# Performance work log

Hardware: AMD Instinct MI355X
Metric: run time of the kernel (lower is better)

Reference implementation:

```python
import jax, jax.numpy as jnp
import numpy as np

B, CIN, COUT, G = 1, 64, 64, 1
NLAT, NLON = 256, 512
LMAX, MMAX = NLAT, NLON // 2 + 1  # torch-harmonics: lmax=nlat, mmax=nlon//2+1


def _legpoly(mmax, lmax, cost):
    """Fully (ortho) normalized associated Legendre \bar P_l^m(cos t), shape [mmax, lmax, nlat]."""
    nlat = cost.shape[0]
    p = np.zeros((mmax, lmax, nlat), dtype=np.float64)
    sint = np.sqrt(1.0 - cost * cost)
    pmm = np.full(nlat, np.sqrt(1.0 / (4.0 * np.pi)))  # \bar P_0^0
    for m in range(mmax):
        if m < lmax:
            p[m, m] = pmm
        if m + 1 < lmax:
            p[m, m + 1] = np.sqrt(2.0 * m + 3.0) * cost * pmm
        for l in range(m + 2, lmax):
            a = np.sqrt((4.0 * l * l - 1.0) / (l * l - m * m))
            b = np.sqrt(((l - 1.0) ** 2 - m * m) / (4.0 * (l - 1.0) ** 2 - 1.0))
            p[m, l] = a * (cost * p[m, l - 1] - b * p[m, l - 2])
        # diagonal step: \bar P_{m+1}^{m+1}
        pmm = -np.sqrt((2.0 * m + 3.0) / (2.0 * m + 2.0)) * sint * pmm
    return p


def setup_inputs():
    key = jax.random.key(0)
    k1, k2, k3 = jax.random.split(key, 3)
    # Gauss-Legendre nodes/weights (grid='legendre-gauss')
    cost, wq = np.polynomial.legendre.leggauss(NLAT)
    pct = _legpoly(MMAX, LMAX, cost)                      # [m, l, k] - ISHT matrix
    sht_w = pct * wq[None, None, :]                        # [m, l, k] - SHT matrix (Legendre * quadrature)
    x = jax.random.normal(k1, (B, CIN, NLAT, NLON), jnp.float32)
    # weight init: scale = sqrt(1/(Cin/g)), scale[0] *= sqrt(2); complex randn has var 1/2 per component
    scale = np.full(LMAX, np.sqrt(1.0 / (CIN // G)), np.float32)
    scale[0] *= np.sqrt(2.0)
    scale = scale * np.sqrt(0.5)
    weight_r = jax.random.normal(k2, (G, CIN // G, COUT // G, LMAX), jnp.float32) * scale
    weight_i = jax.random.normal(k3, (G, CIN // G, COUT // G, LMAX), jnp.float32) * scale
    return {"x": x, "weight_r": weight_r, "weight_i": weight_i,
            "pct": jnp.asarray(pct.astype(np.float32)),
            "sht_w": jnp.asarray(sht_w.astype(np.float32))}


def reference(x, weight_r, weight_i, pct, sht_w):
    residual = x  # scale_residual is False (same in/out shape and grid)
    x = x.astype(jnp.float32)
    # --- forward real SHT: rfft over lon, Legendre transform over lat ---
    xf = 2.0 * jnp.pi * jnp.fft.rfft(x, axis=-1, norm="forward")          # [B,C,k,m] complex64
    coeffs = jnp.einsum('bckm,mlk->bclm', xf, sht_w.astype(xf.dtype))      # [B,C,l,m]
    Bd, C, L, M = coeffs.shape
    # --- grouped per-l complex weight contraction (_contract_lwise) ---
    w = (weight_r + 1j * weight_i).astype(coeffs.dtype)                    # [g,i,o,l]
    xg = coeffs.reshape(Bd, G, C // G, L, M)
    out = jnp.einsum('bgilm,giol->bgolm', xg, w).reshape(Bd, COUT, L, M)
    # --- inverse real SHT ---
    xk = jnp.einsum('bolm,mlk->bokm', out, pct.astype(out.dtype))          # [B,Cout,k,m]
    y = jnp.fft.irfft(xk, n=NLON, axis=-1, norm="forward")                 # [B,Cout,nlat,nlon]
    return (y.astype(residual.dtype), residual)
```

## Files before the change

kernel.cpp:

```cpp
#include <hip/hip_runtime.h>

typedef _Float16 f16;
typedef _Float16 h8 __attribute__((ext_vector_type(8)));
typedef float f4 __attribute__((ext_vector_type(4)));

#define NLON 512
#define NLAT 256
#define NC   64
#define NM   256
#define NL   256
#define RTOT (NC*NLAT)

#define BO_FTR 0
#define BO_FTI (BO_FTR + 262144)
#define BO_GR  (BO_FTI + 262144)
#define BO_GI  (BO_GR  + 262144)
#define BO_WTR (BO_GI  + 262144)
#define BO_WTI (BO_WTR + 2097152)
#define BO_XFRE (BO_WTI + 2097152)
#define BO_XFIM (BO_XFRE + 8388608)
#define BO_PRE  (BO_XFIM + 8388608)
#define BO_PIM  (BO_PRE + 8388608)
#define BO_QRE  (BO_PIM + 8388608)
#define BO_QIM  (BO_QRE + 8388608)

__device__ inline f4 mfma16(h8 a, h8 b, f4 c) {
  return __builtin_amdgcn_mfma_f32_16x16x32_f16(a, b, c, 0, 0, 0);
}

__global__ void k_tables_h(f16* __restrict__ Ftr, f16* __restrict__ Fti,
                           f16* __restrict__ Gr, f16* __restrict__ Gi) {
  int idx = blockIdx.x * blockDim.x + threadIdx.x;
  if (idx >= NLON * NM) return;
  const float step = 3.14159265358979323846f / 256.0f;
  {
    int m = idx >> 9, n = idx & 511;
    int t = (n * m) & (NLON - 1);
    float th = t * step;
    const float sc = 6.2831853071795864769f / 512.0f;
    Ftr[idx] = (f16)(sc * cosf(th));
    Fti[idx] = (f16)(-sc * sinf(th));
  }
  {
    int n = idx >> 8, m = idx & 255;
    int t = (n * m) & (NLON - 1);
    float th = t * step;
    float s = (m == 0) ? 1.0f : 2.0f;
    Gr[idx] = (f16)(s * cosf(th));
    Gi[idx] = (f16)(-s * sinf(th));
  }
}

__global__ void k_permw2(const float* __restrict__ wr, const float* __restrict__ wi,
                         f16* __restrict__ wTr, f16* __restrict__ wTi) {
  __shared__ float tile[32][33];
  int z = blockIdx.z;
  int o = z >> 1;
  const float* w = (z & 1) ? wi : wr;
  f16* wT = (z & 1) ? wTi : wTr;
  int i0 = blockIdx.y * 32;
  int l0 = blockIdx.x * 32;
  int xx = threadIdx.x, yy = threadIdx.y;
  for (int j = 0; j < 32; j += 8)
    tile[yy + j][xx] = w[(size_t)(i0 + yy + j) * (NC * NL) + (size_t)o * NL + l0 + xx];
  __syncthreads();
  for (int j = 0; j < 32; j += 8)
    wT[(size_t)(l0 + yy + j) * (NC * NC) + (size_t)o * NC + i0 + xx] = (f16)tile[xx][yy + j];
}

__global__ __launch_bounds__(256) void k_s1(
    const float* __restrict__ x, const f16* __restrict__ Ftr,
    const f16* __restrict__ Fti, f16* __restrict__ XFre, f16* __restrict__ XFim,
    float* __restrict__ res) {
  __shared__ f16 Ar[128 * 72], Ai[128 * 72], Bx[64 * 72];
  int t = threadIdx.x;
  int m0 = blockIdx.x * 128, r0 = blockIdx.y * 64;
  int lane = t & 63, w = t >> 6;
  int wm = (w >> 1) * 32, wn = (w & 1) * 32;
  int fr = lane & 15, kg = (lane >> 4) * 8;
  int srow = t >> 2, skc = (t & 3) * 16;
  f4 aR[4][2] = {}, aI[4][2] = {};
  for (int n0 = 0; n0 < NLON; n0 += 64) {
#pragma unroll
    for (int rep = 0; rep < 4; ++rep) {
      int f = rep * 256 + t;
      int row = f >> 3, c8 = (f & 7) * 8;
      *(h8*)&Ar[row * 72 + c8] = *(const h8*)(Ftr + (size_t)(m0 + row) * NLON + n0 + c8);
      *(h8*)&Ai[row * 72 + c8] = *(const h8*)(Fti + (size_t)(m0 + row) * NLON + n0 + c8);
    }
    const float* px = x + (size_t)(r0 + srow) * NLON + n0 + skc;
    float4 v0 = *(const float4*)px;
    float4 v1 = *(const float4*)(px + 4);
    float4 v2 = *(const float4*)(px + 8);
    float4 v3 = *(const float4*)(px + 12);
    if (blockIdx.x == 0) {
      float* pr = res + (size_t)(r0 + srow) * NLON + n0 + skc;
      *(float4*)pr = v0; *(float4*)(pr + 4) = v1;
      *(float4*)(pr + 8) = v2; *(float4*)(pr + 12) = v3;
    }
    h8 h0 = {(f16)v0.x, (f16)v0.y, (f16)v0.z, (f16)v0.w,
             (f16)v1.x, (f16)v1.y, (f16)v1.z, (f16)v1.w};
    h8 h1 = {(f16)v2.x, (f16)v2.y, (f16)v2.z, (f16)v2.w,
             (f16)v3.x, (f16)v3.y, (f16)v3.z, (f16)v3.w};
    *(h8*)&Bx[srow * 72 + skc] = h0;
    *(h8*)&Bx[srow * 72 + skc + 8] = h1;
    __syncthreads();
#pragma unroll
    for (int ks = 0; ks < 64; ks += 32) {
      h8 b0 = *(h8*)&Bx[(wn + fr) * 72 + ks + kg];
      h8 b1 = *(h8*)&Bx[(wn + 16 + fr) * 72 + ks + kg];
#pragma unroll
      for (int im = 0; im < 4; ++im) {
        int mrow = wm + (im >> 1) * 64 + (im & 1) * 16 + fr;
        h8 a = *(h8*)&Ar[mrow * 72 + ks + kg];
        h8 c = *(h8*)&Ai[mrow * 72 + ks + kg];
        aR[im][0] = mfma16(a, b0, aR[im][0]); aR[im][1] = mfma16(a, b1, aR[im][1]);
        aI[im][0] = mfma16(c, b0, aI[im][0]); aI[im][1] = mfma16(c, b1, aI[im][1]);
      }
    }
    __syncthreads();
  }
  int drow = (lane >> 4) * 4, dcol = lane & 15;
#pragma unroll
  for (int im = 0; im < 4; ++im)
#pragma unroll
    for (int j = 0; j < 2; ++j)
#pragma unroll
      for (int b = 0; b < 4; ++b) {
        int mg = m0 + wm + (im >> 1) * 64 + (im & 1) * 16 + drow + b;
        size_t o = (size_t)mg * RTOT + r0 + wn + j * 16 + dcol;
        XFre[o] = (f16)aR[im][j][b];
        XFim[o] = (f16)aI[im][j][b];
      }
}

__global__ __launch_bounds__(256) void k_s2(
    const f16* __restrict__ XFre, const f16* __restrict__ XFim,
    const float* __restrict__ shtw, f16* __restrict__ Pre, f16* __restrict__ Pim) {
  int m = blockIdx.y;
  int l0 = blockIdx.x * 64;
  int t = threadIdx.x;
  if (l0 + 64 <= m) return;
  __shared__ f16 SH[9216];
  f16* Ar = SH;
  f16* Ai = SH + 2560;
  f16* Bs = SH + 5120;
  int lane = t & 63, w = t >> 6;
  int wm = (w >> 1) * 32, wn = (w & 1) * 32;
  int fr = lane & 15, kg = (lane >> 4) * 8;
  int srow = t >> 2, skc = (t & 3) * 8;
  const f16* Abr = XFre + (size_t)m * RTOT;
  const f16* Abi = XFim + (size_t)m * RTOT;
  const float* Bb = shtw + (size_t)m * (NL * NLAT);
  f4 aR[2][2] = {}, aI[2][2] = {};
  for (int k0 = 0; k0 < NLAT; k0 += 32) {
    *(h8*)&Ar[srow * 40 + skc] = *(const h8*)(Abr + (size_t)srow * NLAT + k0 + skc);
    *(h8*)&Ai[srow * 40 + skc] = *(const h8*)(Abi + (size_t)srow * NLAT + k0 + skc);
    const float* pb = Bb + (size_t)(l0 + srow) * NLAT + k0 + skc;
    float4 v0 = *(const float4*)pb;
    float4 v1 = *(const float4*)(pb + 4);
    h8 hb = {(f16)v0.x, (f16)v0.y, (f16)v0.z, (f16)v0.w,
             (f16)v1.x, (f16)v1.y, (f16)v1.z, (f16)v1.w};
    *(h8*)&Bs[srow * 40 + skc] = hb;
    __syncthreads();
    h8 a0 = *(h8*)&Ar[(wm + fr) * 40 + kg],      a1 = *(h8*)&Ar[(wm + 16 + fr) * 40 + kg];
    h8 c0 = *(h8*)&Ai[(wm + fr) * 40 + kg],      c1 = *(h8*)&Ai[(wm + 16 + fr) * 40 + kg];
    h8 b0 = *(h8*)&Bs[(wn + fr) * 40 + kg],      b1 = *(h8*)&Bs[(wn + 16 + fr) * 40 + kg];
    aR[0][0] = mfma16(a0, b0, aR[0][0]); aR[0][1] = mfma16(a0, b1, aR[0][1]);
    aR[1][0] = mfma16(a1, b0, aR[1][0]); aR[1][1] = mfma16(a1, b1, aR[1][1]);
    aI[0][0] = mfma16(c0, b0, aI[0][0]); aI[0][1] = mfma16(c0, b1, aI[0][1]);
    aI[1][0] = mfma16(c1, b0, aI[1][0]); aI[1][1] = mfma16(c1, b1, aI[1][1]);
    __syncthreads();
  }
  f16* Tr = SH;
  f16* Ti = SH + 4608;
  int drow = (lane >> 4) * 4, dcol = lane & 15;
#pragma unroll
  for (int i = 0; i < 2; ++i)
#pragma unroll
    for (int j = 0; j < 2; ++j)
#pragma unroll
      for (int b = 0; b < 4; ++b) {
        int c = wm + i * 16 + drow + b;
        int l = wn + j * 16 + dcol;
        Tr[l * 72 + c] = (f16)aR[i][j][b];
        Ti[l * 72 + c] = (f16)aI[i][j][b];
      }
  __syncthreads();
#pragma unroll
  for (int rep = 0; rep < 4; ++rep) {
    int f = rep * 256 + t;
    int buf = f >> 9, idx = f & 511;
    int ll = idx >> 3, c8 = (idx & 7) * 8;
    const f16* T = buf ? Ti : Tr;
    h8 v = *(const h8*)&T[ll * 72 + c8];
    f16* Pd = buf ? Pim : Pre;
    *(h8*)(Pd + (size_t)(l0 + ll) * RTOT + (size_t)m * 64 + c8) = v;
  }
}

__global__ __launch_bounds__(256) void k_s3(
    const f16* __restrict__ Pre, const f16* __restrict__ Pim,
    const f16* __restrict__ wTr, const f16* __restrict__ wTi,
    f16* __restrict__ Qre, f16* __restrict__ Qim) {
  int l = blockIdx.y;
  int m0 = blockIdx.x * 64;
  int t = threadIdx.x;
  size_t obase = (size_t)l * RTOT + (size_t)m0 * 64;
  if (m0 > l) return;
  __shared__ f16 SH[18432];
  f16* Ar = SH;
  f16* Ai = SH + 4608;
  f16* Br = SH + 9216;
  f16* Bi = SH + 13824;
  const f16* Pbr = Pre + (size_t)l * RTOT + (size_t)m0 * 64;
  const f16* Pbi = Pim + (size_t)l * RTOT + (size_t)m0 * 64;
  const f16* Wbr = wTr + (size_t)l * 4096;
  const f16* Wbi = wTi + (size_t)l * 4096;
#pragma unroll
  for (int rep = 0; rep < 2; ++rep) {
    int f = rep * 256 + t;
    int row = f >> 3, c8 = (f & 7) * 8;
    *(h8*)&Ar[row * 72 + c8] = *(const h8*)(Pbr + (size_t)row * 64 + c8);
    *(h8*)&Ai[row * 72 + c8] = *(const h8*)(Pbi + (size_t)row * 64 + c8);
    *(h8*)&Br[row * 72 + c8] = *(const h8*)(Wbr + (size_t)f * 8);
    *(h8*)&Bi[row * 72 + c8] = *(const h8*)(Wbi + (size_t)f * 8);
  }
  __syncthreads();
  int lane = t & 63, w = t >> 6;
  int wm = (w >> 1) * 32, wn = (w & 1) * 32;
  int fr = lane & 15, kg = (lane >> 4) * 8;
  f4 RR[2][2] = {}, II[2][2] = {}, RI[2][2] = {}, IR[2][2] = {};
#pragma unroll
  for (int ks = 0; ks < 64; ks += 32) {
    h8 a0 = *(h8*)&Ar[(wm + fr) * 72 + ks + kg];
    h8 a1 = *(h8*)&Ar[(wm + 16 + fr) * 72 + ks + kg];
    h8 c0 = *(h8*)&Ai[(wm + fr) * 72 + ks + kg];
    h8 c1 = *(h8*)&Ai[(wm + 16 + fr) * 72 + ks + kg];
    h8 b0 = *(h8*)&Br[(wn + fr) * 72 + ks + kg];
    h8 b1 = *(h8*)&Br[(wn + 16 + fr) * 72 + ks + kg];
    h8 d0 = *(h8*)&Bi[(wn + fr) * 72 + ks + kg];
    h8 d1 = *(h8*)&Bi[(wn + 16 + fr) * 72 + ks + kg];
    RR[0][0] = mfma16(a0, b0, RR[0][0]); RR[0][1] = mfma16(a0, b1, RR[0][1]);
    RR[1][0] = mfma16(a1, b0, RR[1][0]); RR[1][1] = mfma16(a1, b1, RR[1][1]);
    II[0][0] = mfma16(c0, d0, II[0][0]); II[0][1] = mfma16(c0, d1, II[0][1]);
    II[1][0] = mfma16(c1, d0, II[1][0]); II[1][1] = mfma16(c1, d1, II[1][1]);
    RI[0][0] = mfma16(a0, d0, RI[0][0]); RI[0][1] = mfma16(a0, d1, RI[0][1]);
    RI[1][0] = mfma16(a1, d0, RI[1][0]); RI[1][1] = mfma16(a1, d1, RI[1][1]);
    IR[0][0] = mfma16(c0, b0, IR[0][0]); IR[0][1] = mfma16(c0, b1, IR[0][1]);
    IR[1][0] = mfma16(c1, b0, IR[1][0]); IR[1][1] = mfma16(c1, b1, IR[1][1]);
  }
  __syncthreads();
  f16* Tr = SH;
  f16* Ti = SH + 4608;
  int drow = (lane >> 4) * 4, dcol = lane & 15;
#pragma unroll
  for (int i = 0; i < 2; ++i)
#pragma unroll
    for (int j = 0; j < 2; ++j)
#pragma unroll
      for (int b = 0; b < 4; ++b) {
        int mm = wm + i * 16 + drow + b;
        int oo = wn + j * 16 + dcol;
        Tr[mm * 72 + oo] = (f16)(RR[i][j][b] - II[i][j][b]);
        Ti[mm * 72 + oo] = (f16)(RI[i][j][b] + IR[i][j][b]);
      }
  __syncthreads();
#pragma unroll
  for (int rep = 0; rep < 4; ++rep) {
    int f = rep * 256 + t;
    int buf = f >> 9, idx = f & 511;
    int mm = idx >> 3, o8 = (idx & 7) * 8;
    const f16* T = buf ? Ti : Tr;
    h8 v = *(const h8*)&T[mm * 72 + o8];
    f16* Qd = buf ? Qim : Qre;
    *(h8*)(Qd + obase + (size_t)mm * 64 + o8) = v;
  }
}

__global__ __launch_bounds__(256) void k_s4(
    const f16* __restrict__ Qre, const f16* __restrict__ Qim,
    const float* __restrict__ pct, f16* __restrict__ XKre, f16* __restrict__ XKim) {
  __shared__ f16 As[32 * 66], Ais[32 * 66], Bs0[32 * 66], Bs1[32 * 66];
  int m = blockIdx.y;
  int k0b = blockIdx.x * 128;
  int t = threadIdx.x;
  int lane = t & 63, w = t >> 6;
  int wm = (w >> 1) * 32, wn = (w & 1) * 32;
  int fr = lane & 15, kg = (lane >> 4) * 8;
  int lr = t >> 3, c8 = (t & 7) * 8;
  const float* Bb = pct + (size_t)m * (NL * NLAT);
  f4 aR[2][4] = {}, aI[2][4] = {};
  int lstart = m & ~31;
  for (int l0 = lstart; l0 < NL; l0 += 32) {
    *(h8*)&As[lr * 66 + c8]  = *(const h8*)(Qre + (size_t)(l0 + lr) * RTOT + (size_t)m * 64 + c8);
    *(h8*)&Ais[lr * 66 + c8] = *(const h8*)(Qim + (size_t)(l0 + lr) * RTOT + (size_t)m * 64 + c8);
    const float* pb = Bb + (size_t)(l0 + lr) * NLAT + k0b + c8;
    {
      float4 v0 = *(const float4*)pb;
      float4 v1 = *(const float4*)(pb + 4);
      h8 hb = {(f16)v0.x, (f16)v0.y, (f16)v0.z, (f16)v0.w,
               (f16)v1.x, (f16)v1.y, (f16)v1.z, (f16)v1.w};
      *(h8*)&Bs0[lr * 66 + c8] = hb;
    }
    {
      float4 v0 = *(const float4*)(pb + 64);
      float4 v1 = *(const float4*)(pb + 68);
      h8 hb = {(f16)v0.x, (f16)v0.y, (f16)v0.z, (f16)v0.w,
               (f16)v1.x, (f16)v1.y, (f16)v1.z, (f16)v1.w};
      *(h8*)&Bs1[lr * 66 + c8] = hb;
    }
    __syncthreads();
    h8 a0, a1, c0, c1, b0, b1, b2, b3;
#pragma unroll
    for (int e = 0; e < 8; ++e) {
      int row = (kg + e) * 66;
      a0[e] = As[row + wm + fr];
      a1[e] = As[row + wm + 16 + fr];
      c0[e] = Ais[row + wm + fr];
      c1[e] = Ais[row + wm + 16 + fr];
      b0[e] = Bs0[row + wn + fr];
      b1[e] = Bs0[row + wn + 16 + fr];
      b2[e] = Bs1[row + wn + fr];
      b3[e] = Bs1[row + wn + 16 + fr];
    }
    aR[0][0] = mfma16(a0, b0, aR[0][0]); aR[0][1] = mfma16(a0, b1, aR[0][1]);
    aR[0][2] = mfma16(a0, b2, aR[0][2]); aR[0][3] = mfma16(a0, b3, aR[0][3]);
    aR[1][0] = mfma16(a1, b0, aR[1][0]); aR[1][1] = mfma16(a1, b1, aR[1][1]);
    aR[1][2] = mfma16(a1, b2, aR[1][2]); aR[1][3] = mfma16(a1, b3, aR[1][3]);
    aI[0][0] = mfma16(c0, b0, aI[0][0]); aI[0][1] = mfma16(c0, b1, aI[0][1]);
    aI[0][2] = mfma16(c0, b2, aI[0][2]); aI[0][3] = mfma16(c0, b3, aI[0][3]);
    aI[1][0] = mfma16(c1, b0, aI[1][0]); aI[1][1] = mfma16(c1, b1, aI[1][1]);
    aI[1][2] = mfma16(c1, b2, aI[1][2]); aI[1][3] = mfma16(c1, b3, aI[1][3]);
    __syncthreads();
  }
  int drow = (lane >> 4) * 4, dcol = lane & 15;
#pragma unroll
  for (int i = 0; i < 2; ++i)
#pragma unroll
    for (int j = 0; j < 4; ++j)
#pragma unroll
      for (int b = 0; b < 4; ++b) {
        int orow = wm + i * 16 + drow + b;
        int kcol = k0b + (j >> 1) * 64 + (j & 1) * 16 + wn + dcol;
        size_t o = (size_t)m * RTOT + (size_t)orow * NLAT + kcol;
        XKre[o] = (f16)aR[i][j][b];
        XKim[o] = (f16)aI[i][j][b];
      }
}

__global__ __launch_bounds__(256) void k_s5(
    const f16* __restrict__ XKre, const f16* __restrict__ XKim,
    const f16* __restrict__ Gr, const f16* __restrict__ Gi,
    float* __restrict__ y) {
  __shared__ f16 Ar[32 * 66], Ai[32 * 66], Br[128 * 34], Bi[128 * 34];
  int t = threadIdx.x;
  int n0 = blockIdx.x * 128, r0 = blockIdx.y * 64;
  int lane = t & 63, w = t >> 6;
  int wm = (w >> 1) * 32, wn = (w & 1) * 32;
  int fr = lane & 15, kg = (lane >> 4) * 8;
  int mr = t >> 3, r8 = (t & 7) * 8;
  f4 acc[2][4] = {};
  for (int m0 = 0; m0 < NM; m0 += 32) {
    *(h8*)&Ar[mr * 66 + r8] = *(const h8*)(XKre + (size_t)(m0 + mr) * RTOT + r0 + r8);
    *(h8*)&Ai[mr * 66 + r8] = *(const h8*)(XKim + (size_t)(m0 + mr) * RTOT + r0 + r8);
#pragma unroll
    for (int rep = 0; rep < 2; ++rep) {
      int f = rep * 256 + t;
      int row = f >> 2, cc = (f & 3) * 8;
      *(h8*)&Br[row * 34 + cc] = *(const h8*)(Gr + (size_t)(n0 + row) * NM + m0 + cc);
      *(h8*)&Bi[row * 34 + cc] = *(const h8*)(Gi + (size_t)(n0 + row) * NM + m0 + cc);
    }
    __syncthreads();
    h8 a0, a1, c0, c1;
#pragma unroll
    for (int e = 0; e < 8; ++e) {
      int row = (kg + e) * 66;
      a0[e] = Ar[row + wm + fr];
      a1[e] = Ar[row + wm + 16 + fr];
      c0[e] = Ai[row + wm + fr];
      c1[e] = Ai[row + wm + 16 + fr];
    }
#pragma unroll
    for (int j = 0; j < 4; ++j) {
      int nb = wn + (j & 1) * 16 + (j >> 1) * 64;
      h8 b = *(h8*)&Br[(nb + fr) * 34 + kg];
      h8 d = *(h8*)&Bi[(nb + fr) * 34 + kg];
      acc[0][j] = mfma16(a0, b, acc[0][j]);
      acc[1][j] = mfma16(a1, b, acc[1][j]);
      acc[0][j] = mfma16(c0, d, acc[0][j]);
      acc[1][j] = mfma16(c1, d, acc[1][j]);
    }
    __syncthreads();
  }
  int drow = (lane >> 4) * 4, dcol = lane & 15;
#pragma unroll
  for (int i = 0; i < 2; ++i)
#pragma unroll
    for (int j = 0; j < 4; ++j)
#pragma unroll
      for (int b = 0; b < 4; ++b) {
        int rg = r0 + wm + i * 16 + drow + b;
        int ng = n0 + wn + (j & 1) * 16 + (j >> 1) * 64 + dcol;
        y[(size_t)rg * NLON + ng] = acc[i][j][b];
      }
}

extern "C" void kernel_launch(void* const* d_in, const int* in_sizes, int n_in,
                              void* d_out, int out_size, void* d_ws, size_t ws_size,
                              hipStream_t stream) {
  const float* x    = (const float*)d_in[0];
  const float* wgr  = (const float*)d_in[1];
  const float* wgi  = (const float*)d_in[2];
  const float* pct  = (const float*)d_in[3];
  const float* shtw = (const float*)d_in[4];
  float* out = (float*)d_out;
  char* ws = (char*)d_ws;

  f16* Ftr = (f16*)(ws + BO_FTR);
  f16* Fti = (f16*)(ws + BO_FTI);
  f16* Gr  = (f16*)(ws + BO_GR);
  f16* Gi  = (f16*)(ws + BO_GI);
  f16* wTr = (f16*)(ws + BO_WTR);
  f16* wTi = (f16*)(ws + BO_WTI);
  f16* XFre = (f16*)(ws + BO_XFRE);
  f16* XFim = (f16*)(ws + BO_XFIM);
  f16* Pre  = (f16*)(ws + BO_PRE);
  f16* Pim  = (f16*)(ws + BO_PIM);
  f16* Qre  = (f16*)(ws + BO_QRE);
  f16* Qim  = (f16*)(ws + BO_QIM);

  float* res = out + (size_t)NC * NLAT * NLON;

  hipLaunchKernelGGL(k_tables_h, dim3(512), dim3(256), 0, stream, Ftr, Fti, Gr, Gi);
  hipLaunchKernelGGL(k_permw2, dim3(8, 2, 128), dim3(32, 8), 0, stream, wgr, wgi, wTr, wTi);
  hipLaunchKernelGGL(k_s1, dim3(2, 256), dim3(256), 0, stream, x, Ftr, Fti, XFre, XFim, res);
  hipLaunchKernelGGL(k_s2, dim3(4, 256), dim3(256), 0, stream, XFre, XFim, shtw, Pre, Pim);
  hipLaunchKernelGGL(k_s3, dim3(4, 256), dim3(256), 0, stream, Pre, Pim, wTr, wTi, Qre, Qim);
  hipLaunchKernelGGL(k_s4, dim3(2, 256), dim3(256), 0, stream, Qre, Qim, pct, XFre, XFim);
  hipLaunchKernelGGL(k_s5, dim3(4, 256), dim3(256), 0, stream, XFre, XFim, Gr, Gi, out);
}
```

Baseline: 130.7 us.

## Stage full K-panel in LDS once and stream other operand directly from global

In the forward DFT, Legendre and inverse DFT kernels, one operand's entire reduction panel is loaded into shared memory once up front. The other operand (DFT or Legendre matrix) is read directly from global memory into MFMA fragments. This removes the per-iteration barriers and shared-memory staging of both operands. The cost is much larger LDS use per block, which may reduce occupancy, and uncoalesced, cache-dependent global fragment loads inside the inner loop.

Result: slower. 160.9 us (+23.1%).

```diff
diff --git a/kernel.cpp b/kernel.cpp
--- a/kernel.cpp
+++ b/kernel.cpp
@@ -72,53 +72,50 @@
     const float* __restrict__ x, const f16* __restrict__ Ftr,
     const f16* __restrict__ Fti, f16* __restrict__ XFre, f16* __restrict__ XFim,
     float* __restrict__ res) {
-  __shared__ f16 Ar[128 * 72], Ai[128 * 72], Bx[64 * 72];
+  __shared__ f16 Bx[64 * 520];
   int t = threadIdx.x;
   int m0 = blockIdx.x * 128, r0 = blockIdx.y * 64;
   int lane = t & 63, w = t >> 6;
   int wm = (w >> 1) * 32, wn = (w & 1) * 32;
   int fr = lane & 15, kg = (lane >> 4) * 8;
-  int srow = t >> 2, skc = (t & 3) * 16;
-  f4 aR[4][2] = {}, aI[4][2] = {};
-  for (int n0 = 0; n0 < NLON; n0 += 64) {
-#pragma unroll
-    for (int rep = 0; rep < 4; ++rep) {
-      int f = rep * 256 + t;
-      int row = f >> 3, c8 = (f & 7) * 8;
-      *(h8*)&Ar[row * 72 + c8] = *(const h8*)(Ftr + (size_t)(m0 + row) * NLON + n0 + c8);
-      *(h8*)&Ai[row * 72 + c8] = *(const h8*)(Fti + (size_t)(m0 + row) * NLON + n0 + c8);
-    }
-    const float* px = x + (size_t)(r0 + srow) * NLON + n0 + skc;
-    float4 v0 = *(const float4*)px;
-    float4 v1 = *(const float4*)(px + 4);
-    float4 v2 = *(const float4*)(px + 8);
-    float4 v3 = *(const float4*)(px + 12);
-    if (blockIdx.x == 0) {
-      float* pr = res + (size_t)(r0 + srow) * NLON + n0 + skc;
-      *(float4*)pr = v0; *(float4*)(pr + 4) = v1;
-      *(float4*)(pr + 8) = v2; *(float4*)(pr + 12) = v3;
+  int srow = t >> 2, sc = (t & 3) * 16;
+  const float* xrow = x + (size_t)(r0 + srow) * NLON;
+  float* rrow = res + (size_t)(r0 + srow) * NLON;
+  bool do_res = (blockIdx.x == 0);
+#pragma unroll
+  for (int rep = 0; rep < 8; ++rep) {
+    int n = rep * 64 + sc;
+    float4 v0 = *(const float4*)(xrow + n);
+    float4 v1 = *(const float4*)(xrow + n + 4);
+    float4 v2 = *(const float4*)(xrow + n + 8);
+    float4 v3 = *(const float4*)(xrow + n + 12);
+    if (do_res) {
+      *(float4*)(rrow + n) = v0; *(float4*)(rrow + n + 4) = v1;
+      *(float4*)(rrow + n + 8) = v2; *(float4*)(rrow + n + 12) = v3;
     }
     h8 h0 = {(f16)v0.x, (f16)v0.y, (f16)v0.z, (f16)v0.w,
              (f16)v1.x, (f16)v1.y, (f16)v1.z, (f16)v1.w};
     h8 h1 = {(f16)v2.x, (f16)v2.y, (f16)v2.z, (f16)v2.w,
              (f16)v3.x, (f16)v3.y, (f16)v3.z, (f16)v3.w};
-    *(h8*)&Bx[srow * 72 + skc] = h0;
-    *(h8*)&Bx[srow * 72 + skc + 8] = h1;
-    __syncthreads();
-#pragma unroll
-    for (int ks = 0; ks < 64; ks += 32) {
-      h8 b0 = *(h8*)&Bx[(wn + fr) * 72 + ks + kg];
-      h8 b1 = *(h8*)&Bx[(wn + 16 + fr) * 72 + ks + kg];
-#pragma unroll
-      for (int im = 0; im < 4; ++im) {
-        int mrow = wm + (im >> 1) * 64 + (im & 1) * 16 + fr;
-        h8 a = *(h8*)&Ar[mrow * 72 + ks + kg];
-        h8 c = *(h8*)&Ai[mrow * 72 + ks + kg];
-        aR[im][0] = mfma16(a, b0, aR[im][0]); aR[im][1] = mfma16(a, b1, aR[im][1]);
-        aI[im][0] = mfma16(c, b0, aI[im][0]); aI[im][1] = mfma16(c, b1, aI[im][1]);
-      }
-    }
-    __syncthreads();
+    *(h8*)&Bx[srow * 520 + n] = h0;
+    *(h8*)&Bx[srow * 520 + n + 8] = h1;
+  }
+  __syncthreads();
+  f4 aR[4][2] = {}, aI[4][2] = {};
+  const f16* Fr0 = Ftr + (size_t)m0 * NLON;
+  const f16* Fi0 = Fti + (size_t)m0 * NLON;
+#pragma unroll 4
+  for (int n0 = 0; n0 < NLON; n0 += 32) {
+    h8 b0 = *(const h8*)&Bx[(wn + fr) * 520 + n0 + kg];
+    h8 b1 = *(const h8*)&Bx[(wn + 16 + fr) * 520 + n0 + kg];
+#pragma unroll
+    for (int im = 0; im < 4; ++im) {
+      int mrow = wm + (im >> 1) * 64 + (im & 1) * 16 + fr;
+      h8 a = *(const h8*)(Fr0 + (size_t)mrow * NLON + n0 + kg);
+      h8 c = *(const h8*)(Fi0 + (size_t)mrow * NLON + n0 + kg);
+      aR[im][0] = mfma16(a, b0, aR[im][0]); aR[im][1] = mfma16(a, b1, aR[im][1]);
+      aI[im][0] = mfma16(c, b0, aI[im][0]); aI[im][1] = mfma16(c, b1, aI[im][1]);
+    }
   }
   int drow = (lane >> 4) * 4, dcol = lane & 15;
 #pragma unroll
@@ -141,37 +138,44 @@
   int l0 = blockIdx.x * 64;
   int t = threadIdx.x;
   if (l0 + 64 <= m) return;
-  __shared__ f16 SH[9216];
-  f16* Ar = SH;
-  f16* Ai = SH + 2560;
-  f16* Bs = SH + 5120;
+  __shared__ f16 SH[2 * 64 * 264];
+  f16* Axr = SH;
+  f16* Axi = SH + 64 * 264;
   int lane = t & 63, w = t >> 6;
   int wm = (w >> 1) * 32, wn = (w & 1) * 32;
   int fr = lane & 15, kg = (lane >> 4) * 8;
-  int srow = t >> 2, skc = (t & 3) * 8;
   const f16* Abr = XFre + (size_t)m * RTOT;
   const f16* Abi = XFim + (size_t)m * RTOT;
+#pragma unroll
+  for (int rep = 0; rep < 8; ++rep) {
+    int f = rep * 256 + t;
+    int row = f >> 5, c8 = (f & 31) * 8;
+    *(h8*)&Axr[row * 264 + c8] = *(const h8*)(Abr + (size_t)row * NLAT + c8);
+    *(h8*)&Axi[row * 264 + c8] = *(const h8*)(Abi + (size_t)row * NLAT + c8);
+  }
+  __syncthreads();
   const float* Bb = shtw + (size_t)m * (NL * NLAT);
   f4 aR[2][2] = {}, aI[2][2] = {};
+#pragma unroll 2
   for (int k0 = 0; k0 < NLAT; k0 += 32) {
-    *(h8*)&Ar[srow * 40 + skc] = *(const h8*)(Abr + (size_t)srow * NLAT + k0 + skc);
-    *(h8*)&Ai[srow * 40 + skc] = *(const h8*)(Abi + (size_t)srow * NLAT + k0 + skc);
-    const float* pb = Bb + (size_t)(l0 + srow) * NLAT + k0 + skc;
-    float4 v0 = *(const float4*)pb;
-    float4 v1 = *(const float4*)(pb + 4);
-    h8 hb = {(f16)v0.x, (f16)v0.y, (f16)v0.z, (f16)v0.w,
-             (f16)v1.x, (f16)v1.y, (f16)v1.z, (f16)v1.w};
-    *(h8*)&Bs[srow * 40 + skc] = hb;
-    __syncthreads();
-    h8 a0 = *(h8*)&Ar[(wm + fr) * 40 + kg],      a1 = *(h8*)&Ar[(wm + 16 + fr) * 40 + kg];
-    h8 c0 = *(h8*)&Ai[(wm + fr) * 40 + kg],      c1 = *(h8*)&Ai[(wm + 16 + fr) * 40 + kg];
-    h8 b0 = *(h8*)&Bs[(wn + fr) * 40 + kg],      b1 = *(h8*)&Bs[(wn + 16 + fr) * 40 + kg];
+    h8 a0 = *(const h8*)&Axr[(wm + fr) * 264 + k0 + kg];
+    h8 a1 = *(const h8*)&Axr[(wm + 16 + fr) * 264 + k0 + kg];
+    h8 c0 = *(const h8*)&Axi[(wm + fr) * 264 + k0 + kg];
+    h8 c1 = *(const h8*)&Axi[(wm + 16 + fr) * 264 + k0 + kg];
+    const float* pb0 = Bb + (size_t)(l0 + wn + fr) * NLAT + k0 + kg;
+    const float* pb1 = Bb + (size_t)(l0 + wn + 16 + fr) * NLAT + k0 + kg;
+    float4 u0 = *(const float4*)pb0, u1 = *(const float4*)(pb0 + 4);
+    float4 u2 = *(const float4*)pb1, u3 = *(const float4*)(pb1 + 4);
+    h8 b0 = {(f16)u0.x, (f16)u0.y, (f16)u0.z, (f16)u0.w,
+             (f16)u1.x, (f16)u1.y, (f16)u1.z, (f16)u1.w};
+    h8 b1 = {(f16)u2.x, (f16)u2.y, (f16)u2.z, (f16)u2.w,
+             (f16)u3.x, (f16)u3.y, (f16)u3.z, (f16)u3.w};
     aR[0][0] = mfma16(a0, b0, aR[0][0]); aR[0][1] = mfma16(a0, b1, aR[0][1]);
     aR[1][0] = mfma16(a1, b0, aR[1][0]); aR[1][1] = mfma16(a1, b1, aR[1][1]);
     aI[0][0] = mfma16(c0, b0, aI[0][0]); aI[0][1] = mfma16(c0, b1, aI[0][1]);
     aI[1][0] = mfma16(c1, b0, aI[1][0]); aI[1][1] = mfma16(c1, b1, aI[1][1]);
-    __syncthreads();
-  }
+  }
+  __syncthreads();
   f16* Tr = SH;
   f16* Ti = SH + 4608;
   int drow = (lane >> 4) * 4, dcol = lane & 15;
@@ -353,45 +357,44 @@
     const f16* __restrict__ XKre, const f16* __restrict__ XKim,
     const f16* __restrict__ Gr, const f16* __restrict__ Gi,
     float* __restrict__ y) {
-  __shared__ f16 Ar[32 * 66], Ai[32 * 66], Br[128 * 34], Bi[128 * 34];
+  __shared__ f16 SH[2 * 256 * 66];
+  f16* Axr = SH;
+  f16* Axi = SH + 256 * 66;
   int t = threadIdx.x;
   int n0 = blockIdx.x * 128, r0 = blockIdx.y * 64;
   int lane = t & 63, w = t >> 6;
   int wm = (w >> 1) * 32, wn = (w & 1) * 32;
   int fr = lane & 15, kg = (lane >> 4) * 8;
-  int mr = t >> 3, r8 = (t & 7) * 8;
+#pragma unroll
+  for (int rep = 0; rep < 8; ++rep) {
+    int f = rep * 256 + t;
+    int row = f >> 3, c8 = (f & 7) * 8;
+    *(h8*)&Axr[row * 66 + c8] = *(const h8*)(XKre + (size_t)row * RTOT + r0 + c8);
+    *(h8*)&Axi[row * 66 + c8] = *(const h8*)(XKim + (size_t)row * RTOT + r0 + c8);
+  }
+  __syncthreads();
   f4 acc[2][4] = {};
+#pragma unroll 2
   for (int m0 = 0; m0 < NM; m0 += 32) {
-    *(h8*)&Ar[mr * 66 + r8] = *(const h8*)(XKre + (size_t)(m0 + mr) * RTOT + r0 + r8);
-    *(h8*)&Ai[mr * 66 + r8] = *(const h8*)(XKim + (size_t)(m0 + mr) * RTOT + r0 + r8);
-#pragma unroll
-    for (int rep = 0; rep < 2; ++rep) {
-      int f = rep * 256 + t;
-      int row = f >> 2, cc = (f & 3) * 8;
-      *(h8*)&Br[row * 34 + cc] = *(const h8*)(Gr + (size_t)(n0 + row) * NM + m0 + cc);
-      *(h8*)&Bi[row * 34 + cc] = *(const h8*)(Gi + (size_t)(n0 + row) * NM + m0 + cc);
-    }
-    __syncthreads();
     h8 a0, a1, c0, c1;
 #pragma unroll
     for (int e = 0; e < 8; ++e) {
-      int row = (kg + e) * 66;
-      a0[e] = Ar[row + wm + fr];
-      a1[e] = Ar[row + wm + 16 + fr];
-      c0[e] = Ai[row + wm + fr];
-      c1[e] = Ai[row + wm + 16 + fr];
+      int row = (m0 + kg + e) * 66;
+      a0[e] = Axr[row + wm + fr];
+      a1[e] = Axr[row + wm + 16 + fr];
+      c0[e] = Axi[row + wm + fr];
+      c1[e] = Axi[row + wm + 16 + fr];
     }
 #pragma unroll
     for (int j = 0; j < 4; ++j) {
       int nb = wn + (j & 1) * 16 + (j >> 1) * 64;
-      h8 b = *(h8*)&Br[(nb + fr) * 34 + kg];
-      h8 d = *(h8*)&Bi[(nb + fr) * 34 + kg];
+      h8 b = *(const h8*)(Gr + (size_t)(n0 + nb + fr) * NM + m0 + kg);
+      h8 d = *(const h8*)(Gi + (size_t)(n0 + nb + fr) * NM + m0 + kg);
       acc[0][j] = mfma16(a0, b, acc[0][j]);
       acc[1][j] = mfma16(a1, b, acc[1][j]);
       acc[0][j] = mfma16(c0, d, acc[0][j]);
       acc[1][j] = mfma16(c1, d, acc[1][j]);
     }
-    __syncthreads();
   }
   int drow = (lane >> 4) * 4, dcol = lane & 15;
 #pragma unroll
```
